# Performance work log

Measured on AMD Instinct MI355X. Metric: run time of the kernel, lower is better.

## Reference

```python
import jax, jax.numpy as jnp
import numpy as np

B, N, IN_DIM = 16, 256, 768
MEM, HID = 300, 64
NEG = -1e30
SLOPE = 0.01  # LeakyReLU negative slope


def setup_inputs() -> dict:
    key = jax.random.key(0)
    ks = jax.random.split(key, 8)
    # binary adjacency mask, float32 as in the torch module's mask_logits math
    adj = (jax.random.uniform(ks[0], (B, N, N)) < 0.3).astype(jnp.float32)
    feature = jax.random.normal(ks[1], (B, N, IN_DIM), jnp.float32)

    def lin(k, fan_in, shape):
        return (jax.random.normal(k, shape, jnp.float32) / np.sqrt(fan_in)).astype(jnp.float32)

    W0 = lin(ks[2], IN_DIM, (IN_DIM, MEM)); b0 = jnp.zeros((MEM,), jnp.float32)
    W1 = lin(ks[3], MEM, (MEM, MEM));       b1 = jnp.zeros((MEM,), jnp.float32)
    A1 = lin(ks[4], 2 * MEM, (2 * MEM, HID)); ab1 = jnp.zeros((HID,), jnp.float32)
    A2 = lin(ks[5], HID, (HID, 1));           ab2 = jnp.zeros((1,), jnp.float32)
    return dict(adj=adj, feature=feature, W0=W0, b0=b0, W1=W1, b1=b1,
                A1=A1, ab1=ab1, A2=A2, ab2=ab2)


def reference(adj, feature, W0, b0, W1, b1, A1, ab1, A2, ab2):
    Bn, Nn = adj.shape[0], adj.shape[1]
    # additive split of the concat-MLP first layer: A1 @ [h_i; h_j] = Wa@h_i + Wb@h_j
    Wa, Wb = A1[:MEM], A1[MEM:]
    a2 = A2[:, 0]
    x = feature
    for Wl, bl in ((W0, b0), (W1, b1)):  # num_layers = 2
        h = x @ Wl + bl                              # [B, N, MEM]
        si = h @ Wa                                  # [B, N, HID] (source half)
        sj = h @ Wb + ab1                            # [B, N, HID] (target half + bias)
        z = jax.nn.relu(si[:, :, None, :] + sj[:, None, :, :])  # [B, N, N, HID]
        e = jnp.einsum('bijh,h->bij', z, a2) + ab2[0]            # [B, N, N]
        e = jnp.where(e > 0, e, SLOPE * e)           # LeakyReLU(0.01)
        logits = e * adj + (1.0 - adj) * NEG         # mask_logits
        # faithful quirk: softmax over the FLATTENED N*N dimension
        att = jax.nn.softmax(logits.reshape(Bn, -1), axis=1).reshape(Bn, Nn, Nn)
        x = jnp.einsum('bij,bjd->bid', att, h)       # bmm aggregation
        # dropout is identity in eval mode
    return x
```

## Files before the change

kernel.cpp:

```cpp
#include <hip/hip_runtime.h>
#include <hip/hip_bf16.h>

static constexpr int Bc = 16;
static constexpr int Nc = 256;
static constexpr float NEGc = -1e30f;
static constexpr float SLOPEc = 0.01f;

using f32x4 = __attribute__((ext_vector_type(4))) float;
using s16x8 = __attribute__((ext_vector_type(8))) short;

__device__ __forceinline__ void mfma16(f32x4& d, s16x8 a, s16x8 b) {
    asm("v_mfma_f32_16x16x32_bf16 %0, %1, %2, %0" : "+v"(d) : "v"(a), "v"(b));
}

__device__ __forceinline__ float wredMax(float v) {
#pragma unroll
    for (int o = 32; o; o >>= 1) v = fmaxf(v, __shfl_xor(v, o, 64));
    return v;
}
__device__ __forceinline__ float wredSum(float v) {
#pragma unroll
    for (int o = 32; o; o >>= 1) v += __shfl_xor(v, o, 64);
    return v;
}

__device__ __forceinline__ unsigned packhi(unsigned u1, unsigned u0) {
    return __builtin_amdgcn_perm(u1, u0, 0x07060302u);
}

__global__ void __launch_bounds__(256) convert_all(
    const float* __restrict__ W0, const float* __restrict__ b0,
    const float* __restrict__ W1, const float* __restrict__ b1,
    const float* __restrict__ A1, const float* __restrict__ ab1,
    ushort* __restrict__ F0h, ushort* __restrict__ F0l,
    ushort* __restrict__ F1h, ushort* __restrict__ F1l,
    float* __restrict__ bias0, float* __restrict__ bias1) {
    int idx = blockIdx.x * 256 + threadIdx.x;
    if (idx >= 79232) return;

    if (idx < 43520) {
        const float* src; ushort *dh, *dl; int K, ch, c;
        if (idx < 30720) { src = W0; dh = F0h; dl = F0l; K = 768;
                           ch = idx / 320; c = idx - ch * 320; }
        else { int off = idx - 30720; src = W1; dh = F1h; dl = F1l; K = 300;
               ch = off / 320; c = off - ch * 320; }
        float v[8];
#pragma unroll
        for (int e = 0; e < 8; e++) {
            int k = ch * 8 + e;
            v[e] = (k < K && c < 300) ? src[(size_t)k * 300 + c] : 0.f;
        }
        unsigned hu[4], lu[4];
#pragma unroll
        for (int q = 0; q < 4; q++) {
            unsigned u0 = __float_as_uint(v[q * 2]);
            unsigned u1 = __float_as_uint(v[q * 2 + 1]);
            float r0 = v[q * 2] - __uint_as_float(u0 & 0xFFFF0000u);
            float r1 = v[q * 2 + 1] - __uint_as_float(u1 & 0xFFFF0000u);
            hu[q] = packhi(u1, u0);
            lu[q] = packhi(__float_as_uint(r1), __float_as_uint(r0));
        }
        size_t dst = ((size_t)ch * 448 + c) * 8;
        *(uint4*)&dh[dst] = make_uint4(hu[0], hu[1], hu[2], hu[3]);
        *(uint4*)&dl[dst] = make_uint4(lu[0], lu[1], lu[2], lu[3]);
    } else if (idx < 78336) {
        const float* Wsrc; ushort *dh, *dl; int K, ch, c, eh;
        if (idx < 68096) {
            int off = idx - 43520; Wsrc = W0; dh = F0h; dl = F0l; K = 768;
            ch = off >> 8; int rem = off & 255; c = rem >> 1; eh = rem & 1;
        } else {
            int off = idx - 68096; Wsrc = W1; dh = F1h; dl = F1l; K = 300;
            ch = off >> 8; int rem = off & 255; c = rem >> 1; eh = rem & 1;
        }
        const float* Wr[4]; float val[4];
#pragma unroll
        for (int i = 0; i < 4; i++) {
            int k = ch * 8 + eh * 4 + i;
            int kc = k < K ? k : 0;
            Wr[i] = Wsrc + (size_t)kc * 300;
            val[i] = (k < K) ? 1.f : 0.f;
        }
        const float* a1c = (c < 64) ? (A1 + c) : (A1 + 300 * 64 + (c - 64));
        float acc[4] = {};
        for (int m = 0; m < 300; m++) {
            float av = a1c[(size_t)m * 64];
#pragma unroll
            for (int i = 0; i < 4; i++) acc[i] += Wr[i][m] * av;
        }
#pragma unroll
        for (int i = 0; i < 4; i++) acc[i] *= val[i];
        unsigned hu[2], lu[2];
#pragma unroll
        for (int q = 0; q < 2; q++) {
            unsigned u0 = __float_as_uint(acc[q * 2]);
            unsigned u1 = __float_as_uint(acc[q * 2 + 1]);
            float r0 = acc[q * 2] - __uint_as_float(u0 & 0xFFFF0000u);
            float r1 = acc[q * 2 + 1] - __uint_as_float(u1 & 0xFFFF0000u);
            hu[q] = packhi(u1, u0);
            lu[q] = packhi(__float_as_uint(r1), __float_as_uint(r0));
        }
        size_t dst = ((size_t)ch * 448 + 320 + c) * 8 + eh * 4;
        *(uint2*)&dh[dst] = make_uint2(hu[0], hu[1]);
        *(uint2*)&dl[dst] = make_uint2(lu[0], lu[1]);
    } else {
        int off = idx - 78336;
        int layer = off / 448, col = off - layer * 448;
        const float* b = layer ? b1 : b0;
        float v;
        if (col < 320) {
            v = (col < 300) ? b[col] : 0.f;
        } else {
            int cc = col - 320;
            const float* a1c = (cc < 64) ? (A1 + cc) : (A1 + 300 * 64 + (cc - 64));
            float s = 0.f;
            for (int m = 0; m < 300; m++) s += b[m] * a1c[(size_t)m * 64];
            v = s + ((cc >= 64) ? ab1[cc - 64] : 0.f);
        }
        (layer ? bias1 : bias0)[col] = v;
    }
}

__global__ void __launch_bounds__(256) mfma_gemm(
    const float* __restrict__ A, long long Abstr, int AS, int Kp,
    const ushort* __restrict__ Wh, const ushort* __restrict__ Wl,
    long long Wbstr, int WCOLS,
    const float* __restrict__ bias,
    float* __restrict__ out, long long Obstr, int OS, int colmax,
    const float* __restrict__ rmx, const float* __restrict__ rsm,
    ushort* __restrict__ TOh, ushort* __restrict__ TOl,
    float* __restrict__ sisjOut) {
    constexpr int BM = 64;
    __shared__ __align__(16) short Ah[2048], Al[2048];
    __shared__ __align__(16) short Bh[2048], Bl[2048];
    __shared__ float sclS[256];
    __shared__ float mb[4], sb[4];

    const int tid = threadIdx.x;
    const int lane = tid & 63, wave = tid >> 6;
    const int wm = wave >> 1, wn = wave & 1;
    const int row0 = blockIdx.y * BM, col0 = blockIdx.x * 64;
    const int bz = blockIdx.z;
    const int m = lane & 15, kch = lane >> 4;

    if (rmx) {
        float mv = rmx[bz * 256 + tid];
        float wmx = wredMax(mv);
        if (!lane) mb[wave] = wmx;
        __syncthreads();
        float M = fmaxf(fmaxf(mb[0], mb[1]), fmaxf(mb[2], mb[3]));
        float ex = expf(mv - M);
        float ws = wredSum(rsm[bz * 256 + tid] * ex);
        if (!lane) sb[wave] = ws;
        __syncthreads();
        float S = sb[0] + sb[1] + sb[2] + sb[3];
        sclS[tid] = ex / S;
    }

    const int arow = tid >> 2;
    const int aoff = (tid & 3) * 8;
    const int bchunk = tid >> 6, bcol = tid & 63;
    const int bsel = (bchunk * 64 + bcol) * 8;

    const float* Ab = A + (size_t)bz * Abstr + (size_t)(row0 + arow) * AS + aoff;
    const ushort* Whb = Wh + (size_t)bz * Wbstr;
    const ushort* Wlb = Wl + (size_t)bz * Wbstr;

    f32x4 acc[2][2];
#pragma unroll
    for (int i = 0; i < 2; i++)
#pragma unroll
        for (int j = 0; j < 2; j++)
#pragma unroll
            for (int e = 0; e < 4; e++) acc[i][j][e] = 0.f;

    float fa[8];
    s16x8 bhv, blv;
    *(float4*)&fa[0] = *(const float4*)(Ab);
    *(float4*)&fa[4] = *(const float4*)(Ab + 4);
    {
        size_t boff = (size_t)bchunk * WCOLS * 8 + (size_t)(col0 + bcol) * 8;
        bhv = *(const s16x8*)(Whb + boff);
        blv = *(const s16x8*)(Wlb + boff);
    }

    for (int k0 = 0; k0 < Kp; k0 += 32) {
        __syncthreads();
#pragma unroll
        for (int q = 0; q < 2; q++) {
            unsigned u0 = __float_as_uint(fa[q * 4 + 0]);
            unsigned u1 = __float_as_uint(fa[q * 4 + 1]);
            unsigned u2 = __float_as_uint(fa[q * 4 + 2]);
            unsigned u3 = __float_as_uint(fa[q * 4 + 3]);
            float r0 = fa[q * 4 + 0] - __uint_as_float(u0 & 0xFFFF0000u);
            float r1 = fa[q * 4 + 1] - __uint_as_float(u1 & 0xFFFF0000u);
            float r2 = fa[q * 4 + 2] - __uint_as_float(u2 & 0xFFFF0000u);
            float r3 = fa[q * 4 + 3] - __uint_as_float(u3 & 0xFFFF0000u);
            uint2 th, tl;
            th.x = packhi(u1, u0); th.y = packhi(u3, u2);
            tl.x = packhi(__float_as_uint(r1), __float_as_uint(r0));
            tl.y = packhi(__float_as_uint(r3), __float_as_uint(r2));
            int kq = aoff + q * 4;
            int base = ((kq >> 3) * BM + arow) * 8 + (kq & 7);
            *(uint2*)&Ah[base] = th;
            *(uint2*)&Al[base] = tl;
        }
        *(s16x8*)&Bh[bsel] = bhv;
        *(s16x8*)&Bl[bsel] = blv;
        __syncthreads();
        if (k0 + 32 < Kp) {
            *(float4*)&fa[0] = *(const float4*)(Ab + k0 + 32);
            *(float4*)&fa[4] = *(const float4*)(Ab + k0 + 36);
            size_t boff = (size_t)(((k0 + 32) >> 3) + bchunk) * WCOLS * 8
                        + (size_t)(col0 + bcol) * 8;
            bhv = *(const s16x8*)(Whb + boff);
            blv = *(const s16x8*)(Wlb + boff);
        }
        s16x8 Afh[2], Afl[2], Bfh[2], Bfl[2];
#pragma unroll
        for (int fr = 0; fr < 2; fr++) {
            int off = (kch * BM + wm * 32 + fr * 16 + m) * 8;
            Afh[fr] = *(const s16x8*)&Ah[off];
            Afl[fr] = *(const s16x8*)&Al[off];
        }
#pragma unroll
        for (int fc = 0; fc < 2; fc++) {
            int off = ((kch << 6) + wn * 32 + fc * 16 + m) * 8;
            Bfh[fc] = *(const s16x8*)&Bh[off];
            Bfl[fc] = *(const s16x8*)&Bl[off];
        }
#pragma unroll
        for (int fr = 0; fr < 2; fr++)
#pragma unroll
            for (int fc = 0; fc < 2; fc++) {
                mfma16(acc[fr][fc], Afh[fr], Bfh[fc]);
                mfma16(acc[fr][fc], Afl[fr], Bfh[fc]);
                mfma16(acc[fr][fc], Afh[fr], Bfl[fc]);
            }
    }
    asm volatile("s_nop 7\ns_nop 7\ns_nop 7" ::);
    float* ob = out ? out + (size_t)bz * Obstr : nullptr;
#pragma unroll
    for (int fr = 0; fr < 2; fr++) {
        int rbase = row0 + wm * 32 + fr * 16 + (kch << 2);
#pragma unroll
        for (int fc = 0; fc < 2; fc++) {
            int col = col0 + wn * 32 + fc * 16 + m;
            float bv = bias ? bias[col] : 0.f;
            float vv[4];
#pragma unroll
            for (int e = 0; e < 4; e++) vv[e] = acc[fr][fc][e] + bv;
            if (rmx) {
#pragma unroll
                for (int e = 0; e < 4; e++) vv[e] *= sclS[(rbase + e) & 255];
            }
            if (sisjOut && col >= 320) {
#pragma unroll
                for (int e = 0; e < 4; e++)
                    sisjOut[(size_t)(rbase + e) * 128 + (col - 320)] = vv[e];
            } else if (TOh) {
                unsigned u0 = __float_as_uint(vv[0]);
                unsigned u1 = __float_as_uint(vv[1]);
                unsigned u2 = __float_as_uint(vv[2]);
                unsigned u3 = __float_as_uint(vv[3]);
                float r0 = vv[0] - __uint_as_float(u0 & 0xFFFF0000u);
                float r1 = vv[1] - __uint_as_float(u1 & 0xFFFF0000u);
                float r2 = vv[2] - __uint_as_float(u2 & 0xFFFF0000u);
                float r3 = vv[3] - __uint_as_float(u3 & 0xFFFF0000u);
                uint2 th, tl;
                th.x = packhi(u1, u0); th.y = packhi(u3, u2);
                tl.x = packhi(__float_as_uint(r1), __float_as_uint(r0));
                tl.y = packhi(__float_as_uint(r3), __float_as_uint(r2));
                int k = rbase & 255, bb = rbase >> 8;
                size_t dst = (size_t)bb * 81920 + ((size_t)(k >> 3) * 320 + col) * 8 + (k & 7);
                *(uint2*)&TOh[dst] = th;
                *(uint2*)&TOl[dst] = tl;
            } else if (ob && col < colmax) {
#pragma unroll
                for (int e = 0; e < 4; e++)
                    ob[(size_t)(rbase + e) * OS + col] = vv[e];
            }
        }
    }
}

__global__ void __launch_bounds__(256) scores_kernel(
    const float* __restrict__ SS,
    const float* __restrict__ adj,
    const float* __restrict__ A2, const float* __restrict__ ab2p,
    float* __restrict__ P, float* __restrict__ rmx, float* __restrict__ rsm) {
    int b = blockIdx.x, ic = blockIdx.y;
    int j = threadIdx.x;
    __shared__ __align__(16) float sis[8][68];
    __shared__ __align__(16) float a2s[64];
    __shared__ __align__(16) float E[8][260];

    if (j < 64) a2s[j] = A2[j];
    for (int idx = j; idx < 8 * 64; idx += 256) {
        int r = idx >> 6, h = idx & 63;
        sis[r][h] = SS[((size_t)b * Nc + ic * 8 + r) * 128 + h];
    }
    __syncthreads();

    float4 sv4[16];
    const float4* sjp = (const float4*)(SS + ((size_t)b * Nc + j) * 128 + 64);
#pragma unroll
    for (int q = 0; q < 16; q++) sv4[q] = sjp[q];
    float acc[8] = {};
    for (int hq = 0; hq < 16; hq++) {
        float4 a2q = *(const float4*)&a2s[hq * 4];
        float4 sjq = sv4[hq];
#pragma unroll
        for (int r = 0; r < 8; r++) {
            float4 siq = *(const float4*)&sis[r][hq * 4];
            acc[r] += a2q.x * fmaxf(siq.x + sjq.x, 0.f)
                    + a2q.y * fmaxf(siq.y + sjq.y, 0.f)
                    + a2q.z * fmaxf(siq.z + sjq.z, 0.f)
                    + a2q.w * fmaxf(siq.w + sjq.w, 0.f);
        }
    }
    float ab2v = ab2p[0];
    const float* adjp = adj + ((size_t)b * Nc + ic * 8) * Nc + j;
#pragma unroll
    for (int r = 0; r < 8; r++) {
        float e = acc[r] + ab2v;
        e = e > 0.f ? e : SLOPEc * e;
        float a = adjp[(size_t)r * Nc];
        E[r][j] = (a != 0.f) ? e : NEGc;
    }
    __syncthreads();
    int wv = j >> 6, lane = j & 63;
#pragma unroll
    for (int rr = 0; rr < 2; rr++) {
        int r = wv * 2 + rr;
        float4 q = *(const float4*)&E[r][lane * 4];
        float m4 = fmaxf(fmaxf(q.x, q.y), fmaxf(q.z, q.w));
        float rm = wredMax(m4);
        float4 p;
        p.x = expf(q.x - rm); p.y = expf(q.y - rm);
        p.z = expf(q.z - rm); p.w = expf(q.w - rm);
        float rs = wredSum(p.x + p.y + p.z + p.w);
        int gi = ic * 8 + r;
        *(float4*)(P + ((size_t)b * Nc + gi) * Nc + lane * 4) = p;
        if (lane == 0) { rmx[b * Nc + gi] = rm; rsm[b * Nc + gi] = rs; }
    }
}

extern "C" void kernel_launch(void* const* d_in, const int* in_sizes, int n_in,
                              void* d_out, int out_size, void* d_ws, size_t ws_size,
                              hipStream_t stream) {
    const float* adj     = (const float*)d_in[0];
    const float* feature = (const float*)d_in[1];
    const float* W0      = (const float*)d_in[2];
    const float* b0      = (const float*)d_in[3];
    const float* W1      = (const float*)d_in[4];
    const float* b1      = (const float*)d_in[5];
    const float* A1      = (const float*)d_in[6];
    const float* ab1     = (const float*)d_in[7];
    const float* A2      = (const float*)d_in[8];
    const float* ab2     = (const float*)d_in[9];

    char* ws = (char*)d_ws;
    float*  x1    = (float*)(ws);
    float*  sisj  = (float*)(ws + 5242880);
    float*  P     = (float*)(ws + 7340032);
    float*  rmx   = (float*)(ws + 11534336);
    float*  rsm   = (float*)(ws + 11550720);
    float*  bias0 = (float*)(ws + 11567104);
    float*  bias1 = (float*)(ws + 11568896);
    ushort* F0h   = (ushort*)(ws + 11570688);
    ushort* F0l   = (ushort*)(ws + 12258816);
    ushort* F1h   = (ushort*)(ws + 12946944);
    ushort* F1l   = (ushort*)(ws + 13233664);
    ushort* Hh    = (ushort*)(ws + 13520384);
    ushort* Hl    = (ushort*)(ws + 16141824);
    float* outp   = (float*)d_out;

    convert_all<<<310, 256, 0, stream>>>(W0, b0, W1, b1, A1, ab1,
                                         F0h, F0l, F1h, F1l, bias0, bias1);

    for (int L = 0; L < 2; L++) {
        const float* X = L ? x1 : feature;
        const ushort* Fh = L ? F1h : F0h;
        const ushort* Fl = L ? F1l : F0l;
        const float* bf = L ? bias1 : bias0;
        int Kp = L ? 320 : 768;
        int AS = L ? 320 : 768;

        mfma_gemm<<<dim3(7, 64, 1), 256, 0, stream>>>(
            X, 0, AS, Kp, Fh, Fl, 0, 448, bf,
            nullptr, 0, 0, 0, nullptr, nullptr, Hh, Hl, sisj);
        scores_kernel<<<dim3(16, 32), 256, 0, stream>>>(
            sisj, adj, A2, ab2, P, rmx, rsm);
        if (L == 0)
            mfma_gemm<<<dim3(5, 4, 16), 256, 0, stream>>>(
                P, 65536, 256, 256, Hh, Hl, 81920, 320, nullptr,
                x1, 81920, 320, 320, rmx, rsm, nullptr, nullptr, nullptr);
        else
            mfma_gemm<<<dim3(5, 4, 16), 256, 0, stream>>>(
                P, 65536, 256, 256, Hh, Hl, 81920, 320, nullptr,
                outp, 76800, 300, 300, rmx, rsm, nullptr, nullptr, nullptr);
    }
}
```

Measured before the change: 103.6 us.

## Fuse all stages into one persistent megakernel with software grid barriers

Replaces the seven separate launches (weight conversion, two projection GEMMs, two score kernels, two P·H GEMMs) with one persistent kernel of 256 blocks. The stages run as job loops separated by atomic-counter grid barriers, which removes launch gaps between stages. It also stores the sj half transposed so each score thread reads 64 strided values instead of contiguous float4s. The risks are spin-wait cost, lower parallelism in stages that have more jobs than 256 blocks (448 and 512 jobs), a deadlock if all blocks are not co-resident, and an extra memset launch.

```diff
diff --git a/kernel.cpp b/kernel.cpp
--- a/kernel.cpp
+++ b/kernel.cpp
@@ -1,10 +1,10 @@
 #include <hip/hip_runtime.h>
 #include <hip/hip_bf16.h>
 
-static constexpr int Bc = 16;
 static constexpr int Nc = 256;
 static constexpr float NEGc = -1e30f;
 static constexpr float SLOPEc = 0.01f;
+static constexpr unsigned NBLK = 256;
 
 using f32x4 = __attribute__((ext_vector_type(4))) float;
 using s16x8 = __attribute__((ext_vector_type(8))) short;
@@ -28,16 +28,26 @@
     return __builtin_amdgcn_perm(u1, u0, 0x07060302u);
 }
 
-__global__ void __launch_bounds__(256) convert_all(
+__device__ __forceinline__ void gridbar(unsigned* cnt, unsigned goal) {
+    __syncthreads();
+    if (threadIdx.x == 0) {
+        __threadfence();
+        atomicAdd(cnt, 1u);
+        while (__hip_atomic_load(cnt, __ATOMIC_RELAXED, __HIP_MEMORY_SCOPE_AGENT) < goal)
+            __builtin_amdgcn_s_sleep(1);
+    }
+    __syncthreads();
+    __threadfence();
+}
+
+__device__ __forceinline__ void convert_item(
+    int idx,
     const float* __restrict__ W0, const float* __restrict__ b0,
     const float* __restrict__ W1, const float* __restrict__ b1,
     const float* __restrict__ A1, const float* __restrict__ ab1,
     ushort* __restrict__ F0h, ushort* __restrict__ F0l,
     ushort* __restrict__ F1h, ushort* __restrict__ F1l,
     float* __restrict__ bias0, float* __restrict__ bias1) {
-    int idx = blockIdx.x * 256 + threadIdx.x;
-    if (idx >= 79232) return;
-
     if (idx < 43520) {
         const float* src; ushort *dh, *dl; int K, ch, c;
         if (idx < 30720) { src = W0; dh = F0h; dl = F0l; K = 768;
@@ -82,10 +92,10 @@
         }
         const float* a1c = (c < 64) ? (A1 + c) : (A1 + 300 * 64 + (c - 64));
         float acc[4] = {};
-        for (int m = 0; m < 300; m++) {
-            float av = a1c[(size_t)m * 64];
-#pragma unroll
-            for (int i = 0; i < 4; i++) acc[i] += Wr[i][m] * av;
+        for (int mm = 0; mm < 300; mm++) {
+            float av = a1c[(size_t)mm * 64];
+#pragma unroll
+            for (int i = 0; i < 4; i++) acc[i] += Wr[i][mm] * av;
         }
 #pragma unroll
         for (int i = 0; i < 4; i++) acc[i] *= val[i];
@@ -113,65 +123,26 @@
             int cc = col - 320;
             const float* a1c = (cc < 64) ? (A1 + cc) : (A1 + 300 * 64 + (cc - 64));
             float s = 0.f;
-            for (int m = 0; m < 300; m++) s += b[m] * a1c[(size_t)m * 64];
+            for (int mm = 0; mm < 300; mm++) s += b[mm] * a1c[(size_t)mm * 64];
             v = s + ((cc >= 64) ? ab1[cc - 64] : 0.f);
         }
         (layer ? bias1 : bias0)[col] = v;
     }
 }
 
-__global__ void __launch_bounds__(256) mfma_gemm(
-    const float* __restrict__ A, long long Abstr, int AS, int Kp,
-    const ushort* __restrict__ Wh, const ushort* __restrict__ Wl,
-    long long Wbstr, int WCOLS,
-    const float* __restrict__ bias,
-    float* __restrict__ out, long long Obstr, int OS, int colmax,
-    const float* __restrict__ rmx, const float* __restrict__ rsm,
-    ushort* __restrict__ TOh, ushort* __restrict__ TOl,
-    float* __restrict__ sisjOut) {
-    constexpr int BM = 64;
-    __shared__ __align__(16) short Ah[2048], Al[2048];
-    __shared__ __align__(16) short Bh[2048], Bl[2048];
-    __shared__ float sclS[256];
-    __shared__ float mb[4], sb[4];
-
+__device__ __forceinline__ void gemm_core(
+    const float* __restrict__ Ab, const ushort* __restrict__ Whb,
+    const ushort* __restrict__ Wlb, int WCOLS, int col0, int Kp,
+    f32x4 (&acc)[2][2]) {
+    __shared__ __align__(16) short Ah[2048], Al[2048], Bh[2048], Bl[2048];
     const int tid = threadIdx.x;
     const int lane = tid & 63, wave = tid >> 6;
     const int wm = wave >> 1, wn = wave & 1;
-    const int row0 = blockIdx.y * BM, col0 = blockIdx.x * 64;
-    const int bz = blockIdx.z;
     const int m = lane & 15, kch = lane >> 4;
-
-    if (rmx) {
-        float mv = rmx[bz * 256 + tid];
-        float wmx = wredMax(mv);
-        if (!lane) mb[wave] = wmx;
-        __syncthreads();
-        float M = fmaxf(fmaxf(mb[0], mb[1]), fmaxf(mb[2], mb[3]));
-        float ex = expf(mv - M);
-        float ws = wredSum(rsm[bz * 256 + tid] * ex);
-        if (!lane) sb[wave] = ws;
-        __syncthreads();
-        float S = sb[0] + sb[1] + sb[2] + sb[3];
-        sclS[tid] = ex / S;
-    }
-
-    const int arow = tid >> 2;
-    const int aoff = (tid & 3) * 8;
+    const int arow = tid >> 2, aoff = (tid & 3) * 8;
     const int bchunk = tid >> 6, bcol = tid & 63;
     const int bsel = (bchunk * 64 + bcol) * 8;
-
-    const float* Ab = A + (size_t)bz * Abstr + (size_t)(row0 + arow) * AS + aoff;
-    const ushort* Whb = Wh + (size_t)bz * Wbstr;
-    const ushort* Wlb = Wl + (size_t)bz * Wbstr;
-
-    f32x4 acc[2][2];
-#pragma unroll
-    for (int i = 0; i < 2; i++)
-#pragma unroll
-        for (int j = 0; j < 2; j++)
-#pragma unroll
-            for (int e = 0; e < 4; e++) acc[i][j][e] = 0.f;
+    (void)arow; (void)aoff;
 
     float fa[8];
     s16x8 bhv, blv;
@@ -199,8 +170,8 @@
             th.x = packhi(u1, u0); th.y = packhi(u3, u2);
             tl.x = packhi(__float_as_uint(r1), __float_as_uint(r0));
             tl.y = packhi(__float_as_uint(r3), __float_as_uint(r2));
-            int kq = aoff + q * 4;
-            int base = ((kq >> 3) * BM + arow) * 8 + (kq & 7);
+            int kq = ((tid & 3) * 8) + q * 4;
+            int base = ((kq >> 3) * 64 + (tid >> 2)) * 8 + (kq & 7);
             *(uint2*)&Ah[base] = th;
             *(uint2*)&Al[base] = tl;
         }
@@ -218,7 +189,7 @@
         s16x8 Afh[2], Afl[2], Bfh[2], Bfl[2];
 #pragma unroll
         for (int fr = 0; fr < 2; fr++) {
-            int off = (kch * BM + wm * 32 + fr * 16 + m) * 8;
+            int off = (kch * 64 + wm * 32 + fr * 16 + m) * 8;
             Afh[fr] = *(const s16x8*)&Ah[off];
             Afl[fr] = *(const s16x8*)&Al[off];
         }
@@ -237,27 +208,39 @@
                 mfma16(acc[fr][fc], Afh[fr], Bfl[fc]);
             }
     }
+}
+
+__device__ __forceinline__ void xf_job(
+    const float* __restrict__ X, int Kp,
+    const ushort* __restrict__ Fh, const ushort* __restrict__ Fl,
+    const float* __restrict__ bias, int row0, int col0,
+    ushort* __restrict__ Hh, ushort* __restrict__ Hl,
+    float* __restrict__ siOut, float* __restrict__ sjT) {
+    const int tid = threadIdx.x;
+    const int lane = tid & 63, wave = tid >> 6;
+    const int wm = wave >> 1, wn = wave & 1;
+    const int m = lane & 15, kch = lane >> 4;
+    f32x4 acc[2][2];
+#pragma unroll
+    for (int i = 0; i < 2; i++)
+#pragma unroll
+        for (int j = 0; j < 2; j++)
+#pragma unroll
+            for (int e = 0; e < 4; e++) acc[i][j][e] = 0.f;
+    const float* Ab = X + (size_t)(row0 + (tid >> 2)) * Kp + (tid & 3) * 8;
+    gemm_core(Ab, Fh, Fl, 448, col0, Kp, acc);
     asm volatile("s_nop 7\ns_nop 7\ns_nop 7" ::);
-    float* ob = out ? out + (size_t)bz * Obstr : nullptr;
 #pragma unroll
     for (int fr = 0; fr < 2; fr++) {
         int rbase = row0 + wm * 32 + fr * 16 + (kch << 2);
 #pragma unroll
         for (int fc = 0; fc < 2; fc++) {
             int col = col0 + wn * 32 + fc * 16 + m;
-            float bv = bias ? bias[col] : 0.f;
+            float bv = bias[col];
             float vv[4];
 #pragma unroll
             for (int e = 0; e < 4; e++) vv[e] = acc[fr][fc][e] + bv;
-            if (rmx) {
-#pragma unroll
-                for (int e = 0; e < 4; e++) vv[e] *= sclS[(rbase + e) & 255];
-            }
-            if (sisjOut && col >= 320) {
-#pragma unroll
-                for (int e = 0; e < 4; e++)
-                    sisjOut[(size_t)(rbase + e) * 128 + (col - 320)] = vv[e];
-            } else if (TOh) {
+            if (col < 320) {
                 unsigned u0 = __float_as_uint(vv[0]);
                 unsigned u1 = __float_as_uint(vv[1]);
                 unsigned u2 = __float_as_uint(vv[2]);
@@ -272,54 +255,108 @@
                 tl.y = packhi(__float_as_uint(r3), __float_as_uint(r2));
                 int k = rbase & 255, bb = rbase >> 8;
                 size_t dst = (size_t)bb * 81920 + ((size_t)(k >> 3) * 320 + col) * 8 + (k & 7);
-                *(uint2*)&TOh[dst] = th;
-                *(uint2*)&TOl[dst] = tl;
-            } else if (ob && col < colmax) {
+                *(uint2*)&Hh[dst] = th;
+                *(uint2*)&Hl[dst] = tl;
+            } else if (col < 384) {
+                int cc = col - 320;
 #pragma unroll
                 for (int e = 0; e < 4; e++)
-                    ob[(size_t)(rbase + e) * OS + col] = vv[e];
+                    siOut[(size_t)(rbase + e) * 64 + cc] = vv[e];
+            } else {
+                int cc = col - 384;
+                int bb = rbase >> 8, j0 = rbase & 255;
+                float4 v4 = make_float4(vv[0], vv[1], vv[2], vv[3]);
+                *(float4*)&sjT[((size_t)(bb * 64 + cc)) * Nc + j0] = v4;
             }
         }
     }
 }
 
-__global__ void __launch_bounds__(256) scores_kernel(
-    const float* __restrict__ SS,
-    const float* __restrict__ adj,
-    const float* __restrict__ A2, const float* __restrict__ ab2p,
-    float* __restrict__ P, float* __restrict__ rmx, float* __restrict__ rsm) {
-    int b = blockIdx.x, ic = blockIdx.y;
-    int j = threadIdx.x;
+__device__ __forceinline__ void pv_job(
+    const float* __restrict__ Pb, const ushort* __restrict__ Hhb,
+    const ushort* __restrict__ Hlb, const float* __restrict__ rmxB,
+    const float* __restrict__ rsmB, int row0, int col0,
+    float* __restrict__ ob, int OS, int colmax) {
+    __shared__ float sclS[256];
+    __shared__ float mb[4], sb[4];
+    const int tid = threadIdx.x;
+    const int lane = tid & 63, wave = tid >> 6;
+    __syncthreads();
+    {
+        float mv = rmxB[tid];
+        float wmx = wredMax(mv);
+        if (!lane) mb[wave] = wmx;
+        __syncthreads();
+        float M = fmaxf(fmaxf(mb[0], mb[1]), fmaxf(mb[2], mb[3]));
+        float ex = expf(mv - M);
+        float ws = wredSum(rsmB[tid] * ex);
+        if (!lane) sb[wave] = ws;
+        __syncthreads();
+        float S = sb[0] + sb[1] + sb[2] + sb[3];
+        sclS[tid] = ex / S;
+    }
+    f32x4 acc[2][2];
+#pragma unroll
+    for (int i = 0; i < 2; i++)
+#pragma unroll
+        for (int j = 0; j < 2; j++)
+#pragma unroll
+            for (int e = 0; e < 4; e++) acc[i][j][e] = 0.f;
+    const float* Ab = Pb + (size_t)(row0 + (tid >> 2)) * Nc + (tid & 3) * 8;
+    gemm_core(Ab, Hhb, Hlb, 320, col0, 256, acc);
+    asm volatile("s_nop 7\ns_nop 7\ns_nop 7" ::);
+    const int wm = wave >> 1, wn = wave & 1;
+    const int m = lane & 15, kch = lane >> 4;
+#pragma unroll
+    for (int fr = 0; fr < 2; fr++) {
+        int rbase = row0 + wm * 32 + fr * 16 + (kch << 2);
+#pragma unroll
+        for (int fc = 0; fc < 2; fc++) {
+            int col = col0 + wn * 32 + fc * 16 + m;
+            if (col < colmax) {
+#pragma unroll
+                for (int e = 0; e < 4; e++)
+                    ob[(size_t)(rbase + e) * OS + col] = acc[fr][fc][e] * sclS[rbase + e];
+            }
+        }
+    }
+}
+
+__device__ __forceinline__ void scores_job(
+    const float* __restrict__ si, const float* __restrict__ sjT,
+    const float* __restrict__ adj, const float* __restrict__ A2, float ab2v,
+    float* __restrict__ P, float* __restrict__ rmx, float* __restrict__ rsm,
+    int b, int ic) {
     __shared__ __align__(16) float sis[8][68];
     __shared__ __align__(16) float a2s[64];
     __shared__ __align__(16) float E[8][260];
-
+    const int j = threadIdx.x;
+    __syncthreads();
     if (j < 64) a2s[j] = A2[j];
-    for (int idx = j; idx < 8 * 64; idx += 256) {
+#pragma unroll
+    for (int idx = j, t = 0; t < 2; t++, idx += 256) {
         int r = idx >> 6, h = idx & 63;
-        sis[r][h] = SS[((size_t)b * Nc + ic * 8 + r) * 128 + h];
-    }
-    __syncthreads();
-
-    float4 sv4[16];
-    const float4* sjp = (const float4*)(SS + ((size_t)b * Nc + j) * 128 + 64);
-#pragma unroll
-    for (int q = 0; q < 16; q++) sv4[q] = sjp[q];
+        sis[r][h] = si[(size_t)(b * Nc + ic * 8 + r) * 64 + h];
+    }
+    float sv[64];
+    const float* sjb = sjT + ((size_t)b << 6) * Nc + j;
+#pragma unroll
+    for (int h = 0; h < 64; h++) sv[h] = sjb[(size_t)h * Nc];
+    __syncthreads();
     float acc[8] = {};
+#pragma unroll
     for (int hq = 0; hq < 16; hq++) {
         float4 a2q = *(const float4*)&a2s[hq * 4];
-        float4 sjq = sv4[hq];
 #pragma unroll
         for (int r = 0; r < 8; r++) {
-            float4 siq = *(const float4*)&sis[r][hq * 4];
-            acc[r] += a2q.x * fmaxf(siq.x + sjq.x, 0.f)
-                    + a2q.y * fmaxf(siq.y + sjq.y, 0.f)
-                    + a2q.z * fmaxf(siq.z + sjq.z, 0.f)
-                    + a2q.w * fmaxf(siq.w + sjq.w, 0.f);
-        }
-    }
-    float ab2v = ab2p[0];
-    const float* adjp = adj + ((size_t)b * Nc + ic * 8) * Nc + j;
+            const float4 siq = *(const float4*)&sis[r][hq * 4];
+            acc[r] += a2q.x * fmaxf(siq.x + sv[hq * 4 + 0], 0.f)
+                    + a2q.y * fmaxf(siq.y + sv[hq * 4 + 1], 0.f)
+                    + a2q.z * fmaxf(siq.z + sv[hq * 4 + 2], 0.f)
+                    + a2q.w * fmaxf(siq.w + sv[hq * 4 + 3], 0.f);
+        }
+    }
+    const float* adjp = adj + (size_t)(b * Nc + ic * 8) * Nc + j;
 #pragma unroll
     for (int r = 0; r < 8; r++) {
         float e = acc[r] + ab2v;
@@ -340,8 +377,59 @@
         p.z = expf(q.z - rm); p.w = expf(q.w - rm);
         float rs = wredSum(p.x + p.y + p.z + p.w);
         int gi = ic * 8 + r;
-        *(float4*)(P + ((size_t)b * Nc + gi) * Nc + lane * 4) = p;
+        *(float4*)(P + (size_t)(b * Nc + gi) * Nc + lane * 4) = p;
         if (lane == 0) { rmx[b * Nc + gi] = rm; rsm[b * Nc + gi] = rs; }
+    }
+}
+
+__global__ void __launch_bounds__(256) gat_mega(
+    const float* __restrict__ adj, const float* __restrict__ feature,
+    const float* __restrict__ W0, const float* __restrict__ b0,
+    const float* __restrict__ W1, const float* __restrict__ b1,
+    const float* __restrict__ A1, const float* __restrict__ ab1,
+    const float* __restrict__ A2, const float* __restrict__ ab2,
+    float* __restrict__ outp, float* __restrict__ x1,
+    float* __restrict__ si, float* __restrict__ sjT,
+    float* __restrict__ P, float* __restrict__ rmx, float* __restrict__ rsm,
+    float* __restrict__ bias0, float* __restrict__ bias1,
+    ushort* __restrict__ F0h, ushort* __restrict__ F0l,
+    ushort* __restrict__ F1h, ushort* __restrict__ F1l,
+    ushort* __restrict__ Hh, ushort* __restrict__ Hl,
+    unsigned* __restrict__ barcnt) {
+    const int bid = blockIdx.x;
+    const int tid = threadIdx.x;
+
+    for (int idx = bid * 256 + tid; idx < 79232; idx += 65536)
+        convert_item(idx, W0, b0, W1, b1, A1, ab1,
+                     F0h, F0l, F1h, F1l, bias0, bias1);
+    gridbar(barcnt, 1 * NBLK);
+
+    const float ab2v = ab2[0];
+    for (int L = 0; L < 2; L++) {
+        const float* X = L ? x1 : feature;
+        const ushort* Fh = L ? F1h : F0h;
+        const ushort* Fl = L ? F1l : F0l;
+        const float* bf = L ? bias1 : bias0;
+        const int Kp = L ? 320 : 768;
+
+        for (int job = bid; job < 448; job += NBLK)
+            xf_job(X, Kp, Fh, Fl, bf, (job / 7) * 64, (job % 7) * 64,
+                   Hh, Hl, si, sjT);
+        gridbar(barcnt, (2 + 3 * L) * NBLK);
+
+        for (int job = bid; job < 512; job += NBLK)
+            scores_job(si, sjT, adj, A2, ab2v, P, rmx, rsm, job >> 5, job & 31);
+        gridbar(barcnt, (3 + 3 * L) * NBLK);
+
+        float* ob = L ? outp : x1;
+        const int OS = L ? 300 : 320;
+        for (int job = bid; job < 320; job += NBLK) {
+            int c = job % 5, t = job / 5, r = t & 3, b = t >> 2;
+            pv_job(P + (size_t)b * 65536, Hh + (size_t)b * 81920,
+                   Hl + (size_t)b * 81920, rmx + b * 256, rsm + b * 256,
+                   r * 64, c * 64, ob + (size_t)b * 256 * OS, OS, OS);
+        }
+        if (L == 0) gridbar(barcnt, 4 * NBLK);
     }
 }
 
@@ -361,7 +449,8 @@
 
     char* ws = (char*)d_ws;
     float*  x1    = (float*)(ws);
-    float*  sisj  = (float*)(ws + 5242880);
+    float*  si    = (float*)(ws + 5242880);
+    float*  sjT   = (float*)(ws + 6291456);
     float*  P     = (float*)(ws + 7340032);
     float*  rmx   = (float*)(ws + 11534336);
     float*  rsm   = (float*)(ws + 11550720);
@@ -373,31 +462,12 @@
     ushort* F1l   = (ushort*)(ws + 13233664);
     ushort* Hh    = (ushort*)(ws + 13520384);
     ushort* Hl    = (ushort*)(ws + 16141824);
+    unsigned* bar = (unsigned*)(ws + 18763264);
     float* outp   = (float*)d_out;
 
-    convert_all<<<310, 256, 0, stream>>>(W0, b0, W1, b1, A1, ab1,
-                                         F0h, F0l, F1h, F1l, bias0, bias1);
-
-    for (int L = 0; L < 2; L++) {
-        const float* X = L ? x1 : feature;
-        const ushort* Fh = L ? F1h : F0h;
-        const ushort* Fl = L ? F1l : F0l;
-        const float* bf = L ? bias1 : bias0;
-        int Kp = L ? 320 : 768;
-        int AS = L ? 320 : 768;
-
-        mfma_gemm<<<dim3(7, 64, 1), 256, 0, stream>>>(
-            X, 0, AS, Kp, Fh, Fl, 0, 448, bf,
-            nullptr, 0, 0, 0, nullptr, nullptr, Hh, Hl, sisj);
-        scores_kernel<<<dim3(16, 32), 256, 0, stream>>>(
-            sisj, adj, A2, ab2, P, rmx, rsm);
-        if (L == 0)
-            mfma_gemm<<<dim3(5, 4, 16), 256, 0, stream>>>(
-                P, 65536, 256, 256, Hh, Hl, 81920, 320, nullptr,
-                x1, 81920, 320, 320, rmx, rsm, nullptr, nullptr, nullptr);
-        else
-            mfma_gemm<<<dim3(5, 4, 16), 256, 0, stream>>>(
-                P, 65536, 256, 256, Hh, Hl, 81920, 320, nullptr,
-                outp, 76800, 300, 300, rmx, rsm, nullptr, nullptr, nullptr);
-    }
-}
+    hipMemsetAsync(bar, 0, 64, stream);
+    gat_mega<<<dim3(NBLK), dim3(256), 0, stream>>>(
+        adj, feature, W0, b0, W1, b1, A1, ab1, A2, ab2,
+        outp, x1, si, sjT, P, rmx, rsm, bias0, bias1,
+        F0h, F0l, F1h, F1l, Hh, Hl, bar);
+}
```

Measured after the change: 336.5 us. +224.7%, slower.
